# Performance work log

Hardware: AMD Instinct MI355X
Metric: run time of the kernel (lower is better)

Reference implementation:

```python
import jax, jax.numpy as jnp
import numpy as np
from jax import lax

UNITS = 128
NUM_STEPS = 2048
BATCH = 32
MIN_OMEGA = 0.1
MAX_OMEGA = 70.1
DT = 1.0 / 173.61          # EEG sampling interval
INPUT_SCALER = 0.1
BETA = 0.01
TWO_PI = 2 * 3.1415        # module uses 3.1415, not math.pi


def setup_inputs() -> dict:
    key = jax.random.key(0)
    k1, k2 = jax.random.split(key)
    X_r = jax.random.normal(k1, (BATCH, NUM_STEPS, UNITS), dtype=jnp.float32)
    X_i = jax.random.normal(k2, (BATCH, NUM_STEPS, UNITS), dtype=jnp.float32)
    omegas = (jnp.linspace(MIN_OMEGA, MAX_OMEGA, UNITS) * TWO_PI).astype(jnp.float32)[None, :]  # [1, U]
    return {"X_r": X_r, "X_i": X_i, "omegas": omegas}


def reference(X_r, X_i, omegas):
    B, T, U = X_r.shape
    r0 = jnp.ones((B, U), dtype=X_r.dtype)
    phi0 = jnp.zeros((B, U), dtype=X_r.dtype)

    def step(carry, xs):
        r, phi = carry
        xr, xi = xs  # [B, U] each
        input_r = INPUT_SCALER * xr * jnp.cos(phi)
        input_phi = INPUT_SCALER * xi * jnp.sin(phi)
        r = r + ((1.0 - BETA * jnp.square(r)) * r + input_r) * DT
        phi = phi + (omegas - input_phi) * DT
        return (r, phi), (r, phi)

    xs = (jnp.transpose(X_r, (1, 0, 2)), jnp.transpose(X_i, (1, 0, 2)))  # [T, B, U]
    _, (r_seq, phi_seq) = lax.scan(step, (r0, phi0), xs)
    r = jnp.transpose(r_seq, (1, 0, 2))    # [B, T, U]
    phi = jnp.transpose(phi_seq, (1, 0, 2))
    z_real = r * jnp.cos(phi)
    z_imag = r * jnp.sin(phi)
    return (z_real, z_imag)
```

## Files before the change

### kernel.cpp

```cpp
#include <hip/hip_runtime.h>
#include <math.h>

namespace {
constexpr int kUnits = 128;
constexpr int kSteps = 2048;
constexpr int kBatch = 32;
constexpr int kSeg = 16;
constexpr int kNSeg = kSteps / kSeg;
constexpr int kUBlk = 16;
constexpr int kUPT = 2;
constexpr int kUG = kUBlk / kUPT;
constexpr int kThreads = kUG * kNSeg;
constexpr int kBlocks = kBatch * (kUnits / kUBlk);
constexpr int kGrp = 16;
constexpr int kGrpSeg = kNSeg / kGrp;
constexpr int kPad = kUBlk + 1;
constexpr double kDT = 1.0 / 173.61;
constexpr double kTwoPi = 6.283185307179586;
constexpr double kInv2Pi = 1.0 / kTwoPi;
constexpr size_t kChainElems = (size_t)kSteps * kUnits;

typedef float v2f __attribute__((ext_vector_type(2)));

struct Tables {
  float G[kSteps];
  float Gseg[kNSeg];
  float Gg[kGrp];
  float rbar0[kNSeg];
};
constexpr Tables make_tables() {
  Tables tb{};
  double r = 1.0;
  for (int t = 0; t < kSteps; ++t) {
    if (t % kSeg == 0) tb.rbar0[t / kSeg] = (float)r;
    tb.G[t] = (float)(1.0 + (1.0 - 0.03 * r * r) * kDT);
    r = r + (1.0 - 0.01 * r * r) * r * kDT;
  }
  for (int s = 0; s < kNSeg; ++s) {
    double p = 1.0;
    for (int j = 0; j < kSeg; ++j) p *= (double)tb.G[s * kSeg + j];
    tb.Gseg[s] = (float)p;
  }
  for (int g = 0; g < kGrp; ++g) {
    double p = 1.0;
    for (int s = 0; s < kGrpSeg; ++s) p *= (double)tb.Gseg[g * kGrpSeg + s];
    tb.Gg[g] = (float)p;
  }
  return tb;
}
}

__constant__ Tables kTab = make_tables();

__global__ __launch_bounds__(kThreads)
void hopf_fused(const float* __restrict__ Xr, const float* __restrict__ Xi,
                const float* __restrict__ Om,
                float* __restrict__ Zr, float* __restrict__ Zi) {
  __shared__ float sG[kNSeg][kPad];
  __shared__ float sH[kNSeg][kPad];
  __shared__ float sP[kNSeg][kPad];
  __shared__ float sQ[kNSeg][kPad];
  __shared__ float cG[kGrp][kPad], cH[kGrp][kPad], cP[kGrp][kPad], cQ[kGrp][kPad];
  __shared__ float pD[kGrp][kPad], pR[kGrp][kPad];

  const int tid = threadIdx.x;
  const int ug = tid & (kUG - 1);
  const int seg = tid >> 3;
  const int b = blockIdx.x >> 3;
  const int uq = blockIdx.x & 7;
  const int u0 = uq * kUBlk + ug * kUPT;
  const int t0 = seg * kSeg;

  float cw[kUPT], sw[kUPT], c0[kUPT], s0[kUPT];
  double wdt_d[kUPT];
#pragma unroll
  for (int k = 0; k < kUPT; ++k) {
    const double wdt = (double)Om[u0 + k] * kDT;
    wdt_d[k] = wdt;
    double sd, cd;
    sincos(wdt, &sd, &cd);
    cw[k] = (float)cd;
    sw[k] = (float)sd;
    const double ang = wdt * (double)t0;
    const double kk = rint(ang * kInv2Pi);
    const float th = (float)fma(-kk, kTwoPi, ang);
    __sincosf(th, &s0[k], &c0[k]);
  }

  const size_t base = ((size_t)b * kSteps + t0) * (size_t)kUnits + u0;
  const v2f* xr2 = (const v2f*)(Xr + base);
  const v2f* xi2 = (const v2f*)(Xi + base);
  v2f xr[kSeg], xi[kSeg];
#pragma unroll
  for (int j = 0; j < kSeg; ++j) {
    xr[j] = xr2[j * (kUnits / 2)];
    xi[j] = xi2[j * (kUnits / 2)];
  }

  const float cdt = (float)(0.1 * kDT);
  float gr[kUPT] = {1.f, 1.f}, hr[kUPT] = {0.f, 0.f};
  float pr[kUPT] = {0.f, 0.f}, qr[kUPT] = {0.f, 0.f};
#pragma unroll
  for (int j = 0; j < kSeg; ++j) {
    const float Ge = kTab.G[t0 + j];
#pragma unroll
    for (int k = 0; k < kUPT; ++k) {
      const float axi = cdt * xi[j][k];
      const float axr = cdt * xr[j][k];
      const float ge = fmaf(-axi, c0[k], 1.f);
      const float he = -axi * s0[k];
      const float pe = -axr * s0[k];
      const float qe = axr * c0[k];
      const float g2 = gr[k] * ge;
      const float h2 = fmaf(ge, hr[k], he);
      const float p2 = fmaf(pe, gr[k], Ge * pr[k]);
      const float q2 = fmaf(pe, hr[k], fmaf(Ge, qr[k], qe));
      gr[k] = g2; hr[k] = h2; pr[k] = p2; qr[k] = q2;
      const float c1 = fmaf(cw[k], c0[k], -(sw[k] * s0[k]));
      const float s1 = fmaf(cw[k], s0[k], sw[k] * c0[k]);
      c0[k] = c1; s0[k] = s1;
    }
  }
#pragma unroll
  for (int k = 0; k < kUPT; ++k) {
    const int ch = ug * kUPT + k;
    sG[seg][ch] = gr[k];
    sH[seg][ch] = hr[k];
    sP[seg][ch] = pr[k];
    sQ[seg][ch] = qr[k];
  }
  __syncthreads();

  if (tid < kUBlk * kGrp) {
    const int ch = tid & (kUBlk - 1);
    const int gb = tid >> 4;
    float g = 1.f, h = 0.f, p = 0.f, q = 0.f;
#pragma unroll
    for (int i = 0; i < kGrpSeg; ++i) {
      const int sg = gb * kGrpSeg + i;
      const float mg = sG[sg][ch], mh = sH[sg][ch];
      const float mp = sP[sg][ch], mq = sQ[sg][ch];
      const float Gs = kTab.Gseg[sg];
      const float g2 = mg * g;
      const float h2 = fmaf(mg, h, mh);
      const float p2 = fmaf(mp, g, Gs * p);
      const float q2 = fmaf(mp, h, fmaf(Gs, q, mq));
      g = g2; h = h2; p = p2; q = q2;
    }
    cG[gb][ch] = g; cH[gb][ch] = h; cP[gb][ch] = p; cQ[gb][ch] = q;
  }
  __syncthreads();

  if (tid < kUBlk) {
    const int ch = tid;
    float d = 0.f, rho = 0.f;
#pragma unroll
    for (int gb = 0; gb < kGrp; ++gb) {
      pD[gb][ch] = d;
      pR[gb][ch] = rho;
      const float g = cG[gb][ch], h = cH[gb][ch];
      const float p = cP[gb][ch], q = cQ[gb][ch];
      const float Gs = kTab.Gg[gb];
      const float dn = fmaf(g, d, h);
      const float rn = fmaf(p, d, fmaf(Gs, rho, q));
      d = dn; rho = rn;
    }
  }
  __syncthreads();

  if (tid < kUBlk * kGrp) {
    const int ch = tid & (kUBlk - 1);
    const int gb = tid >> 4;
    float d = pD[gb][ch], rho = pR[gb][ch];
#pragma unroll
    for (int i = 0; i < kGrpSeg; ++i) {
      const int sg = gb * kGrpSeg + i;
      const float mg = sG[sg][ch], mh = sH[sg][ch];
      const float mp = sP[sg][ch], mq = sQ[sg][ch];
      sG[sg][ch] = d;
      sH[sg][ch] = rho;
      const float Gs = kTab.Gseg[sg];
      const float dn = fmaf(mg, d, mh);
      const float rn = fmaf(mp, d, fmaf(Gs, rho, mq));
      d = dn; rho = rn;
    }
  }
  __syncthreads();

  float c[kUPT], s[kUPT], r[kUPT];
#pragma unroll
  for (int k = 0; k < kUPT; ++k) {
    const int ch = ug * kUPT + k;
    const float delta = sG[seg][ch];
    const float rho = sH[seg][ch];
    const double ang = wdt_d[k] * (double)t0 + (double)delta;
    const double kk = rint(ang * kInv2Pi);
    const float th = (float)fma(-kk, kTwoPi, ang);
    __sincosf(th, &s[k], &c[k]);
    r[k] = kTab.rbar0[seg] + rho;
  }

  const float DTf = (float)kDT;
  const float nscale = -(0.1f * DTf);
  const float c01dt = 0.1f * DTf;
  v2f* zr2 = (v2f*)(Zr + base);
  v2f* zi2 = (v2f*)(Zi + base);
#pragma unroll
  for (int j = 0; j < kSeg; ++j) {
    v2f ozr, ozi;
#pragma unroll
    for (int k = 0; k < kUPT; ++k) {
      const float eps = (xi[j][k] * nscale) * s[k];
      const float A = fmaf(-sw[k], eps, cw[k]);
      const float B = fmaf(cw[k], eps, sw[k]);
      const float c2 = fmaf(A, c[k], -(B * s[k]));
      const float s2 = fmaf(A, s[k], B * c[k]);
      const float rr = r[k] * r[k];
      const float om1 = fmaf(-0.01f, rr, 1.f);
      const float racc = fmaf(xr[j][k] * c[k], c01dt, r[k]);
      r[k] = fmaf(om1 * r[k], DTf, racc);
      c[k] = c2; s[k] = s2;
      ozr[k] = r[k] * c[k];
      ozi[k] = r[k] * s[k];
    }
    __builtin_nontemporal_store(ozr, &zr2[j * (kUnits / 2)]);
    __builtin_nontemporal_store(ozi, &zi2[j * (kUnits / 2)]);
  }
}

extern "C" void kernel_launch(void* const* d_in, const int* in_sizes, int n_in,
                              void* d_out, int out_size, void* d_ws, size_t ws_size,
                              hipStream_t stream) {
  const float* Xr = (const float*)d_in[0];
  const float* Xi = (const float*)d_in[1];
  const float* Om = (const float*)d_in[2];
  float* Zr = (float*)d_out;
  float* Zi = (float*)d_out + (size_t)kBatch * kChainElems;

  hipLaunchKernelGGL(hopf_fused, dim3(kBlocks), dim3(kThreads), 0, stream,
                     Xr, Xi, Om, Zr, Zi);
}
```

Measured before the change: 122.8 us.

## Split fused scan kernel into scan and replay kernels via workspace

Splits the single fused kernel into two launches. The first computes per-segment linearized transforms, scans them and writes per-segment start phase offsets and radii to a workspace. The second reloads the inputs with 4-wide vectors and replays the recurrence to write outputs. The scan kernel no longer holds the inputs in registers across barriers, which should free registers and raise occupancy. The cost is a second read of X, an extra launch and a workspace round trip.

```diff
diff --git a/kernel.cpp b/kernel.cpp
--- a/kernel.cpp
+++ b/kernel.cpp
@@ -10,17 +10,23 @@
 constexpr int kUBlk = 16;
 constexpr int kUPT = 2;
 constexpr int kUG = kUBlk / kUPT;
-constexpr int kThreads = kUG * kNSeg;
-constexpr int kBlocks = kBatch * (kUnits / kUBlk);
+constexpr int kThreads1 = kUG * kNSeg;
+constexpr int kBlocks1 = kBatch * (kUnits / kUBlk);
 constexpr int kGrp = 16;
 constexpr int kGrpSeg = kNSeg / kGrp;
 constexpr int kPad = kUBlk + 1;
+constexpr int kUPT2 = 4;
+constexpr int kNQ = kUnits / kUPT2;
+constexpr int kThreads2 = 256;
+constexpr int kItems2 = kBatch * kNSeg * kNQ;
+constexpr int kBlocks2 = kItems2 / kThreads2;
 constexpr double kDT = 1.0 / 173.61;
 constexpr double kTwoPi = 6.283185307179586;
 constexpr double kInv2Pi = 1.0 / kTwoPi;
 constexpr size_t kChainElems = (size_t)kSteps * kUnits;
 
 typedef float v2f __attribute__((ext_vector_type(2)));
+typedef float v4f __attribute__((ext_vector_type(4)));
 
 struct Tables {
   float G[kSteps];
@@ -52,10 +58,9 @@
 
 __constant__ Tables kTab = make_tables();
 
-__global__ __launch_bounds__(kThreads)
-void hopf_fused(const float* __restrict__ Xr, const float* __restrict__ Xi,
-                const float* __restrict__ Om,
-                float* __restrict__ Zr, float* __restrict__ Zi) {
+__global__ __launch_bounds__(kThreads1, 4)
+void hopf_scan(const float* __restrict__ Xr, const float* __restrict__ Xi,
+               const float* __restrict__ Om, float* __restrict__ Ws) {
   __shared__ float sG[kNSeg][kPad];
   __shared__ float sH[kNSeg][kPad];
   __shared__ float sP[kNSeg][kPad];
@@ -72,11 +77,9 @@
   const int t0 = seg * kSeg;
 
   float cw[kUPT], sw[kUPT], c0[kUPT], s0[kUPT];
-  double wdt_d[kUPT];
 #pragma unroll
   for (int k = 0; k < kUPT; ++k) {
     const double wdt = (double)Om[u0 + k] * kDT;
-    wdt_d[k] = wdt;
     double sd, cd;
     sincos(wdt, &sd, &cd);
     cw[k] = (float)cd;
@@ -90,23 +93,18 @@
   const size_t base = ((size_t)b * kSteps + t0) * (size_t)kUnits + u0;
   const v2f* xr2 = (const v2f*)(Xr + base);
   const v2f* xi2 = (const v2f*)(Xi + base);
-  v2f xr[kSeg], xi[kSeg];
-#pragma unroll
-  for (int j = 0; j < kSeg; ++j) {
-    xr[j] = xr2[j * (kUnits / 2)];
-    xi[j] = xi2[j * (kUnits / 2)];
-  }
-
   const float cdt = (float)(0.1 * kDT);
   float gr[kUPT] = {1.f, 1.f}, hr[kUPT] = {0.f, 0.f};
   float pr[kUPT] = {0.f, 0.f}, qr[kUPT] = {0.f, 0.f};
 #pragma unroll
   for (int j = 0; j < kSeg; ++j) {
+    const v2f xrj = xr2[j * (kUnits / 2)];
+    const v2f xij = xi2[j * (kUnits / 2)];
     const float Ge = kTab.G[t0 + j];
 #pragma unroll
     for (int k = 0; k < kUPT; ++k) {
-      const float axi = cdt * xi[j][k];
-      const float axr = cdt * xr[j][k];
+      const float axi = cdt * xij[k];
+      const float axr = cdt * xrj[k];
       const float ge = fmaf(-axi, c0[k], 1.f);
       const float he = -axi * s0[k];
       const float pe = -axr * s0[k];
@@ -187,29 +185,71 @@
   }
   __syncthreads();
 
-  float c[kUPT], s[kUPT], r[kUPT];
-#pragma unroll
-  for (int k = 0; k < kUPT; ++k) {
-    const int ch = ug * kUPT + k;
-    const float delta = sG[seg][ch];
-    const float rho = sH[seg][ch];
-    const double ang = wdt_d[k] * (double)t0 + (double)delta;
+  {
+    const int ch = ug * kUPT;
+    const float d0 = sG[seg][ch], r0 = kTab.rbar0[seg] + sH[seg][ch];
+    const float d1 = sG[seg][ch + 1], r1 = kTab.rbar0[seg] + sH[seg][ch + 1];
+    v4f s4; s4[0] = d0; s4[1] = r0; s4[2] = d1; s4[3] = r1;
+    v4f* w4 = (v4f*)Ws;
+    w4[(size_t)(b * kNSeg + seg) * (kUnits / 2) + uq * kUG + ug] = s4;
+  }
+}
+
+__global__ __launch_bounds__(kThreads2, 2)
+void hopf_replay(const float* __restrict__ Xr, const float* __restrict__ Xi,
+                 const float* __restrict__ Om, const float* __restrict__ Ws,
+                 float* __restrict__ Zr, float* __restrict__ Zi) {
+  const int gid = blockIdx.x * kThreads2 + threadIdx.x;
+  const int up = gid & (kNQ - 1);
+  const int bs = gid >> 5;
+  const int seg = bs & (kNSeg - 1);
+  const int b = bs >> 7;
+  const int u0 = up * kUPT2;
+  const int t0 = seg * kSeg;
+
+  const v4f* w4 = (const v4f*)Ws;
+  const size_t sIdx = (size_t)(b * kNSeg + seg) * (kUnits / 2) + up * 2;
+  const v4f sA = w4[sIdx];
+  const v4f sB = w4[sIdx + 1];
+  const v4f om = *(const v4f*)(Om + u0);
+
+  float cw[kUPT2], sw[kUPT2], c[kUPT2], s[kUPT2], r[kUPT2];
+  const float dl[kUPT2] = {sA[0], sA[2], sB[0], sB[2]};
+  const float rs[kUPT2] = {sA[1], sA[3], sB[1], sB[3]};
+#pragma unroll
+  for (int k = 0; k < kUPT2; ++k) {
+    const double wdt = (double)om[k] * kDT;
+    double sd, cd;
+    sincos(wdt, &sd, &cd);
+    cw[k] = (float)cd;
+    sw[k] = (float)sd;
+    const double ang = wdt * (double)t0 + (double)dl[k];
     const double kk = rint(ang * kInv2Pi);
     const float th = (float)fma(-kk, kTwoPi, ang);
     __sincosf(th, &s[k], &c[k]);
-    r[k] = kTab.rbar0[seg] + rho;
+    r[k] = rs[k];
+  }
+
+  const size_t base = ((size_t)b * kSteps + t0) * (size_t)kUnits + u0;
+  const v4f* xr4 = (const v4f*)(Xr + base);
+  const v4f* xi4 = (const v4f*)(Xi + base);
+  v4f xr[kSeg], xi[kSeg];
+#pragma unroll
+  for (int j = 0; j < kSeg; ++j) {
+    xr[j] = xr4[j * (kUnits / 4)];
+    xi[j] = xi4[j * (kUnits / 4)];
   }
 
   const float DTf = (float)kDT;
   const float nscale = -(0.1f * DTf);
   const float c01dt = 0.1f * DTf;
-  v2f* zr2 = (v2f*)(Zr + base);
-  v2f* zi2 = (v2f*)(Zi + base);
+  v4f* zr4 = (v4f*)(Zr + base);
+  v4f* zi4 = (v4f*)(Zi + base);
 #pragma unroll
   for (int j = 0; j < kSeg; ++j) {
-    v2f ozr, ozi;
-#pragma unroll
-    for (int k = 0; k < kUPT; ++k) {
+    v4f ozr, ozi;
+#pragma unroll
+    for (int k = 0; k < kUPT2; ++k) {
       const float eps = (xi[j][k] * nscale) * s[k];
       const float A = fmaf(-sw[k], eps, cw[k]);
       const float B = fmaf(cw[k], eps, sw[k]);
@@ -223,8 +263,8 @@
       ozr[k] = r[k] * c[k];
       ozi[k] = r[k] * s[k];
     }
-    __builtin_nontemporal_store(ozr, &zr2[j * (kUnits / 2)]);
-    __builtin_nontemporal_store(ozi, &zi2[j * (kUnits / 2)]);
+    __builtin_nontemporal_store(ozr, &zr4[j * (kUnits / 4)]);
+    __builtin_nontemporal_store(ozi, &zi4[j * (kUnits / 4)]);
   }
 }
 
@@ -236,7 +276,10 @@
   const float* Om = (const float*)d_in[2];
   float* Zr = (float*)d_out;
   float* Zi = (float*)d_out + (size_t)kBatch * kChainElems;
-
-  hipLaunchKernelGGL(hopf_fused, dim3(kBlocks), dim3(kThreads), 0, stream,
-                     Xr, Xi, Om, Zr, Zi);
-}
+  float* Ws = (float*)d_ws;
+
+  hipLaunchKernelGGL(hopf_scan, dim3(kBlocks1), dim3(kThreads1), 0, stream,
+                     Xr, Xi, Om, Ws);
+  hipLaunchKernelGGL(hopf_replay, dim3(kBlocks2), dim3(kThreads2), 0, stream,
+                     Xr, Xi, Om, Ws, Zr, Zi);
+}
```

Result: slower. 134.8 us (+9.7%).

## Use 4-wide unit vectors with shorter segments and reload inputs instead of caching

Applied to the files above, without the earlier changes.

Segment length drops from 16 to 8 and units per thread rise from 2 to 4, so each thread issues 128-bit loads and stores. Inputs are no longer held in registers across the scan; they are read again from global memory in the output pass. The final phase reconstruction now rotates the cached start-of-segment sincos by the correction angle, which removes the double-precision range reduction. A launch-bounds occupancy hint is also added. The costs are double the global input reads and shorter segments, which make the shared-memory scan do more work relative to the per-segment chains.

```diff
diff --git a/kernel.cpp b/kernel.cpp
--- a/kernel.cpp
+++ b/kernel.cpp
@@ -5,10 +5,10 @@
 constexpr int kUnits = 128;
 constexpr int kSteps = 2048;
 constexpr int kBatch = 32;
-constexpr int kSeg = 16;
+constexpr int kSeg = 8;
 constexpr int kNSeg = kSteps / kSeg;
 constexpr int kUBlk = 16;
-constexpr int kUPT = 2;
+constexpr int kUPT = 4;
 constexpr int kUG = kUBlk / kUPT;
 constexpr int kThreads = kUG * kNSeg;
 constexpr int kBlocks = kBatch * (kUnits / kUBlk);
@@ -20,7 +20,7 @@
 constexpr double kInv2Pi = 1.0 / kTwoPi;
 constexpr size_t kChainElems = (size_t)kSteps * kUnits;
 
-typedef float v2f __attribute__((ext_vector_type(2)));
+typedef float v4f __attribute__((ext_vector_type(4)));
 
 struct Tables {
   float G[kSteps];
@@ -52,7 +52,7 @@
 
 __constant__ Tables kTab = make_tables();
 
-__global__ __launch_bounds__(kThreads)
+__global__ __launch_bounds__(kThreads, 4)
 void hopf_fused(const float* __restrict__ Xr, const float* __restrict__ Xi,
                 const float* __restrict__ Om,
                 float* __restrict__ Zr, float* __restrict__ Zi) {
@@ -65,18 +65,17 @@
 
   const int tid = threadIdx.x;
   const int ug = tid & (kUG - 1);
-  const int seg = tid >> 3;
+  const int seg = tid >> 2;
   const int b = blockIdx.x >> 3;
   const int uq = blockIdx.x & 7;
   const int u0 = uq * kUBlk + ug * kUPT;
   const int t0 = seg * kSeg;
 
-  float cw[kUPT], sw[kUPT], c0[kUPT], s0[kUPT];
-  double wdt_d[kUPT];
+  const v4f om4 = *(const v4f*)(Om + u0);
+  float cw[kUPT], sw[kUPT], c0[kUPT], s0[kUPT], c0i[kUPT], s0i[kUPT];
 #pragma unroll
   for (int k = 0; k < kUPT; ++k) {
-    const double wdt = (double)Om[u0 + k] * kDT;
-    wdt_d[k] = wdt;
+    const double wdt = (double)om4[k] * kDT;
     double sd, cd;
     sincos(wdt, &sd, &cd);
     cw[k] = (float)cd;
@@ -85,28 +84,25 @@
     const double kk = rint(ang * kInv2Pi);
     const float th = (float)fma(-kk, kTwoPi, ang);
     __sincosf(th, &s0[k], &c0[k]);
+    c0i[k] = c0[k];
+    s0i[k] = s0[k];
   }
 
   const size_t base = ((size_t)b * kSteps + t0) * (size_t)kUnits + u0;
-  const v2f* xr2 = (const v2f*)(Xr + base);
-  const v2f* xi2 = (const v2f*)(Xi + base);
-  v2f xr[kSeg], xi[kSeg];
+  const v4f* xr4 = (const v4f*)(Xr + base);
+  const v4f* xi4 = (const v4f*)(Xi + base);
+  const float cdt = (float)(0.1 * kDT);
+  float gr[kUPT] = {1.f, 1.f, 1.f, 1.f}, hr[kUPT] = {0.f, 0.f, 0.f, 0.f};
+  float pr[kUPT] = {0.f, 0.f, 0.f, 0.f}, qr[kUPT] = {0.f, 0.f, 0.f, 0.f};
 #pragma unroll
   for (int j = 0; j < kSeg; ++j) {
-    xr[j] = xr2[j * (kUnits / 2)];
-    xi[j] = xi2[j * (kUnits / 2)];
-  }
-
-  const float cdt = (float)(0.1 * kDT);
-  float gr[kUPT] = {1.f, 1.f}, hr[kUPT] = {0.f, 0.f};
-  float pr[kUPT] = {0.f, 0.f}, qr[kUPT] = {0.f, 0.f};
-#pragma unroll
-  for (int j = 0; j < kSeg; ++j) {
+    const v4f xrj = xr4[j * (kUnits / 4)];
+    const v4f xij = xi4[j * (kUnits / 4)];
     const float Ge = kTab.G[t0 + j];
 #pragma unroll
     for (int k = 0; k < kUPT; ++k) {
-      const float axi = cdt * xi[j][k];
-      const float axr = cdt * xr[j][k];
+      const float axi = cdt * xij[k];
+      const float axr = cdt * xrj[k];
       const float ge = fmaf(-axi, c0[k], 1.f);
       const float he = -axi * s0[k];
       const float pe = -axr * s0[k];
@@ -193,38 +189,40 @@
     const int ch = ug * kUPT + k;
     const float delta = sG[seg][ch];
     const float rho = sH[seg][ch];
-    const double ang = wdt_d[k] * (double)t0 + (double)delta;
-    const double kk = rint(ang * kInv2Pi);
-    const float th = (float)fma(-kk, kTwoPi, ang);
-    __sincosf(th, &s[k], &c[k]);
+    float sd, cd;
+    __sincosf(delta, &sd, &cd);
+    c[k] = fmaf(c0i[k], cd, -(s0i[k] * sd));
+    s[k] = fmaf(s0i[k], cd, c0i[k] * sd);
     r[k] = kTab.rbar0[seg] + rho;
   }
 
   const float DTf = (float)kDT;
   const float nscale = -(0.1f * DTf);
   const float c01dt = 0.1f * DTf;
-  v2f* zr2 = (v2f*)(Zr + base);
-  v2f* zi2 = (v2f*)(Zi + base);
+  v4f* zr4 = (v4f*)(Zr + base);
+  v4f* zi4 = (v4f*)(Zi + base);
 #pragma unroll
   for (int j = 0; j < kSeg; ++j) {
-    v2f ozr, ozi;
+    const v4f xrj = xr4[j * (kUnits / 4)];
+    const v4f xij = xi4[j * (kUnits / 4)];
+    v4f ozr, ozi;
 #pragma unroll
     for (int k = 0; k < kUPT; ++k) {
-      const float eps = (xi[j][k] * nscale) * s[k];
+      const float eps = (xij[k] * nscale) * s[k];
       const float A = fmaf(-sw[k], eps, cw[k]);
       const float B = fmaf(cw[k], eps, sw[k]);
       const float c2 = fmaf(A, c[k], -(B * s[k]));
       const float s2 = fmaf(A, s[k], B * c[k]);
       const float rr = r[k] * r[k];
       const float om1 = fmaf(-0.01f, rr, 1.f);
-      const float racc = fmaf(xr[j][k] * c[k], c01dt, r[k]);
+      const float racc = fmaf(xrj[k] * c[k], c01dt, r[k]);
       r[k] = fmaf(om1 * r[k], DTf, racc);
       c[k] = c2; s[k] = s2;
       ozr[k] = r[k] * c[k];
       ozi[k] = r[k] * s[k];
     }
-    __builtin_nontemporal_store(ozr, &zr2[j * (kUnits / 2)]);
-    __builtin_nontemporal_store(ozi, &zi2[j * (kUnits / 2)]);
+    __builtin_nontemporal_store(ozr, &zr4[j * (kUnits / 4)]);
+    __builtin_nontemporal_store(ozi, &zi4[j * (kUnits / 4)]);
   }
 }
 
```

Measured after the change: 141.9 us. 15.6% more time.
